# Kernel optimization log

Hardware: AMD Instinct MI355X
Metric: run time of the kernel (lower is better)

The kernel has to match this reference:

```python
import jax, jax.numpy as jnp
import numpy as np

B, C, LO, LQ, H = 64, 4, 64, 128, 768
NEG = -10000.0


def _trilinear(u, um, v, vm, w1, b1, w2, b2, w3):
    # u: [N, Lu, H], v: [N, Lv, H]; returns [N, Lu, Lv]
    p1 = u @ w1 + b1                                  # [N, Lu, 1]
    p2 = (v @ w2 + b2).transpose(0, 2, 1)             # [N, 1, Lv]
    p3 = jnp.einsum('bud,bvd->buv', u * w3, v)        # trilinear term
    return p1 + p2 + p3 + ((1.0 - um) * NEG)[:, :, None] + ((1.0 - vm) * NEG)[:, None, :]


def _forward(encoded_o, encoded_q, om, qm,
             att_W1_w, att_W1_b, att_W2_w, att_W2_b, att_W3,
             Wc_self_w, Wc_self_b, Wc_w, Wc_b, Va_w, Va_b, Wg_w, Wg_b,
             co_W1_w, co_W1_b, co_W2_w, co_W2_b, co_W3, Wp_w, Wp_b,
             sa_W1_w, sa_W1_b, sa_W2_w, sa_W2_b, sa_W3, Wf_w, Wf_b):
    b, c, lo, h = encoded_o.shape
    lq = encoded_q.shape[2]
    p = c * (c - 1)
    # ---- pairwise option-compare (OCN_Att_layer) over all (i, j), j != i ----
    i_idx = np.repeat(np.arange(c), c - 1)
    j_idx = np.array([j for i in range(c) for j in range(c) if j != i])
    o_i = encoded_o[:, i_idx].reshape(b * p, lo, h)   # 'ok'
    o_j = encoded_o[:, j_idx].reshape(b * p, lo, h)   # 'ol'
    m_i = om[:, i_idx].reshape(b * p, lo)
    m_j = om[:, j_idx].reshape(b * p, lo)
    A = _trilinear(o_j, m_j, o_i, m_i, att_W1_w, att_W1_b, att_W2_w, att_W2_b, att_W3)
    att = jax.nn.softmax(A, axis=1)
    olk_ctx = jnp.einsum('bud,buv->bvd', o_j, att)    # [BP, LO, H]
    OLK = jnp.concatenate([o_i - olk_ctx, o_i * olk_ctx], axis=-1)  # [BP, LO, 2H]
    cmp_proj = OLK @ Wc_w + Wc_b                      # Wc applied per compare pair
    cmp_sum = cmp_proj.reshape(b, c, c - 1, lo, h).sum(axis=2).reshape(b * c, lo, h)
    # ---- merge layer (per candidate, flattened into batch) ----
    o1 = encoded_o.reshape(b * c, lo, h)
    q = encoded_q.reshape(b * c, lq, h)
    omf = om.reshape(b * c, lo)
    qmf = qm.reshape(b * c, lq)
    Aq = jax.nn.softmax(q @ Va_w + Va_b + ((1.0 - qmf) * NEG)[:, :, None], axis=1)  # [BC, LQ, 1]
    Q = jnp.einsum('bld,blo->bod', q, Aq)             # [BC, 1, H]
    OCK = jnp.tanh(o1 @ Wc_self_w + Wc_self_b + cmp_sum)
    Qb = jnp.broadcast_to(Q, (b * c, lo, h))
    G = jax.nn.sigmoid(jnp.concatenate([o1, OCK, Qb], axis=-1) @ Wg_w + Wg_b)
    merged = G * o1 + (1.0 - G) * OCK                 # [BC, LO, H]
    # ---- co-attention with question ----
    A2 = _trilinear(q, qmf, merged, omf, co_W1_w, co_W1_b, co_W2_w, co_W2_b, co_W3)  # [BC, LQ, LO]
    ACK = jax.nn.softmax(A2, axis=2)
    OA = jnp.einsum('bqo,bod->bqd', ACK, merged)      # [BC, LQ, H]
    APK = jax.nn.softmax(A2, axis=1)
    dOA = jnp.concatenate([q, OA], axis=-1)           # [BC, LQ, 2H]
    POAA = jnp.einsum('bqd,bqo->bod', dOA, APK)       # [BC, LO, 2H]
    OPK = jax.nn.relu(jnp.concatenate([merged, POAA], axis=-1) @ Wp_w + Wp_b)
    # ---- self-attention ----
    A3 = _trilinear(OPK, omf, OPK, omf, sa_W1_w, sa_W1_b, sa_W2_w, sa_W2_b, sa_W3)
    att3 = jax.nn.softmax(A3, axis=1)
    OSK = jnp.einsum('bud,buv->bvd', OPK, att3)
    OFK = jax.nn.relu(jnp.concatenate([OPK, OSK, OPK - OSK, OPK * OSK], axis=-1) @ Wf_w + Wf_b)
    return OFK.reshape(b, c, lo, h).max(axis=2)       # [B, C, H]


def setup_inputs():
    ks = jax.random.split(jax.random.key(0), 32)
    def p(i, shape, s=0.02):
        return jax.random.normal(ks[i], shape, jnp.float32) * s
    return {
        'encoded_o': jax.random.normal(ks[0], (B, C, LO, H), jnp.float32),
        'encoded_q': jax.random.normal(ks[1], (B, C, LQ, H), jnp.float32),
        'option_mask': jnp.ones((B, C, LO), jnp.int32),
        'question_mask': jnp.ones((B, C, LQ), jnp.int32),
        'att_W1_w': p(2, (H, 1)), 'att_W1_b': p(3, (1,)),
        'att_W2_w': p(4, (H, 1)), 'att_W2_b': p(5, (1,)),
        'att_W3': p(6, (H,)),
        'Wc_self_w': p(7, (H, H)), 'Wc_self_b': p(8, (H,)),
        'Wc_w': p(9, (2 * H, H)), 'Wc_b': p(10, (H,)),
        'Va_w': p(11, (H, 1)), 'Va_b': p(12, (1,)),
        'Wg_w': p(13, (3 * H, H)), 'Wg_b': p(14, (H,)),
        'co_W1_w': p(15, (H, 1)), 'co_W1_b': p(16, (1,)),
        'co_W2_w': p(17, (H, 1)), 'co_W2_b': p(18, (1,)),
        'co_W3': p(19, (H,)),
        'Wp_w': p(20, (3 * H, H)), 'Wp_b': p(21, (H,)),
        'sa_W1_w': p(22, (H, 1)), 'sa_W1_b': p(23, (1,)),
        'sa_W2_w': p(24, (H, 1)), 'sa_W2_b': p(25, (1,)),
        'sa_W3': p(26, (H,)),
        'Wf_w': p(27, (4 * H, H)), 'Wf_b': p(28, (H,)),
    }


def reference(encoded_o, encoded_q, option_mask, question_mask,
              att_W1_w, att_W1_b, att_W2_w, att_W2_b, att_W3,
              Wc_self_w, Wc_self_b, Wc_w, Wc_b, Va_w, Va_b, Wg_w, Wg_b,
              co_W1_w, co_W1_b, co_W2_w, co_W2_b, co_W3, Wp_w, Wp_b,
              sa_W1_w, sa_W1_b, sa_W2_w, sa_W2_b, sa_W3, Wf_w, Wf_b):
    return _forward(encoded_o, encoded_q,
                    option_mask.astype(jnp.float32), question_mask.astype(jnp.float32),
                    att_W1_w, att_W1_b, att_W2_w, att_W2_b, att_W3,
                    Wc_self_w, Wc_self_b, Wc_w, Wc_b, Va_w, Va_b, Wg_w, Wg_b,
                    co_W1_w, co_W1_b, co_W2_w, co_W2_b, co_W3, Wp_w, Wp_b,
                    sa_W1_w, sa_W1_b, sa_W2_w, sa_W2_b, sa_W3, Wf_w, Wf_b)
```

## Files before the change

kernel.cpp:

```cpp
#include <hip/hip_runtime.h>
#include <math.h>


#define NEGC (-10000.0f)
constexpr int HD = 768;
constexpr int KSTR = 9216;

constexpr int EP_TANH = 1;
constexpr int EP_MERGE = 2;
constexpr int EP_RELU = 3;
constexpr int EP_RELU_MAX = 4;

typedef __attribute__((ext_vector_type(8))) short bf16x8;
typedef __attribute__((ext_vector_type(8))) unsigned short u16x8;
typedef __attribute__((ext_vector_type(4))) unsigned short u16x4;
typedef __attribute__((ext_vector_type(4))) float f32x4;

__device__ inline void st8(float* dst, float4 a0, float4 a1) {
  dst[0] = a0.x; dst[1] = a0.y; dst[2] = a0.z; dst[3] = a0.w;
  dst[4] = a1.x; dst[5] = a1.y; dst[6] = a1.z; dst[7] = a1.w;
}

__device__ inline unsigned short f2bf(float x) {
  unsigned int u = __float_as_uint(x);
  u += 0x7fffu + ((u >> 16) & 1u);
  return (unsigned short)(u >> 16);
}

__device__ inline float bf2f(unsigned short u) {
  return __uint_as_float(((unsigned int)u) << 16);
}

__device__ inline u16x8 pack8(float4 a, float4 b) {
  u16x8 r;
  r[0] = f2bf(a.x); r[1] = f2bf(a.y); r[2] = f2bf(a.z); r[3] = f2bf(a.w);
  r[4] = f2bf(b.x); r[5] = f2bf(b.y); r[6] = f2bf(b.z); r[7] = f2bf(b.w);
  return r;
}

__device__ inline u16x4 pack4(float4 a) {
  u16x4 r;
  r[0] = f2bf(a.x); r[1] = f2bf(a.y); r[2] = f2bf(a.z); r[3] = f2bf(a.w);
  return r;
}

__device__ inline void gload_lds16(const unsigned short* src, unsigned short* dst) {
  __builtin_amdgcn_global_load_lds(
      (const __attribute__((address_space(1))) void*)src,
      (__attribute__((address_space(3))) void*)dst, 16, 0, 0);
}

__global__ __launch_bounds__(256)
void bfprep_dot_kernel(const float* __restrict__ x, const float* __restrict__ w3,
                       const float* __restrict__ w1, const float* __restrict__ b1,
                       const float* __restrict__ w2, const float* __restrict__ b2,
                       unsigned short* __restrict__ xbf, unsigned short* __restrict__ xw3,
                       float* __restrict__ o1, float* __restrict__ o2, int ntok) {
  int tok = blockIdx.x * 4 + (threadIdx.x >> 6);
  int lane = threadIdx.x & 63;
  if (tok >= ntok) return;
  const float* xp = x + (size_t)tok * HD;
  unsigned short* xb = xbf + (size_t)tok * HD;
  unsigned short* xw = xw3 + (size_t)tok * HD;
  float s1 = 0.f, s2 = 0.f;
#pragma unroll
  for (int i = 0; i < 3; ++i) {
    int c = (lane + (i << 6)) << 2;
    float4 xv = *(const float4*)(xp + c);
    float4 w3v = *(const float4*)(w3 + c);
    float4 wa = *(const float4*)(w1 + c);
    float4 wb = *(const float4*)(w2 + c);
    s1 = fmaf(xv.x, wa.x, s1); s1 = fmaf(xv.y, wa.y, s1);
    s1 = fmaf(xv.z, wa.z, s1); s1 = fmaf(xv.w, wa.w, s1);
    s2 = fmaf(xv.x, wb.x, s2); s2 = fmaf(xv.y, wb.y, s2);
    s2 = fmaf(xv.z, wb.z, s2); s2 = fmaf(xv.w, wb.w, s2);
    *(u16x4*)(xb + c) = pack4(xv);
    float4 sv;
    sv.x = xv.x * w3v.x; sv.y = xv.y * w3v.y; sv.z = xv.z * w3v.z; sv.w = xv.w * w3v.w;
    *(u16x4*)(xw + c) = pack4(sv);
  }
#pragma unroll
  for (int off = 32; off; off >>= 1) {
    s1 += __shfl_xor(s1, off);
    s2 += __shfl_xor(s2, off);
  }
  if (lane == 0) { o1[tok] = s1 + b1[0]; o2[tok] = s2 + b2[0]; }
}

__global__ __launch_bounds__(256)
void opkprep_kernel(const unsigned short* __restrict__ x, const float* __restrict__ w3,
                    const float* __restrict__ w1, const float* __restrict__ b1,
                    const float* __restrict__ w2, const float* __restrict__ b2,
                    unsigned short* __restrict__ xw3,
                    float* __restrict__ o1, float* __restrict__ o2, int ntok) {
  int tok = blockIdx.x * 4 + (threadIdx.x >> 6);
  int lane = threadIdx.x & 63;
  if (tok >= ntok) return;
  const unsigned short* xp = x + (size_t)tok * HD;
  unsigned short* xw = xw3 + (size_t)tok * HD;
  float s1 = 0.f, s2 = 0.f;
#pragma unroll
  for (int i = 0; i < 3; ++i) {
    int c = (lane + (i << 6)) << 2;
    u16x4 xv = *(const u16x4*)(xp + c);
    float x0 = bf2f(xv[0]), x1 = bf2f(xv[1]), x2 = bf2f(xv[2]), x3 = bf2f(xv[3]);
    float4 w3v = *(const float4*)(w3 + c);
    float4 wa = *(const float4*)(w1 + c);
    float4 wb = *(const float4*)(w2 + c);
    s1 = fmaf(x0, wa.x, s1); s1 = fmaf(x1, wa.y, s1);
    s1 = fmaf(x2, wa.z, s1); s1 = fmaf(x3, wa.w, s1);
    s2 = fmaf(x0, wb.x, s2); s2 = fmaf(x1, wb.y, s2);
    s2 = fmaf(x2, wb.z, s2); s2 = fmaf(x3, wb.w, s2);
    u16x4 sv;
    sv[0] = f2bf(x0 * w3v.x); sv[1] = f2bf(x1 * w3v.y);
    sv[2] = f2bf(x2 * w3v.z); sv[3] = f2bf(x3 * w3v.w);
    *(u16x4*)(xw + c) = sv;
  }
#pragma unroll
  for (int off = 32; off; off >>= 1) {
    s1 += __shfl_xor(s1, off);
    s2 += __shfl_xor(s2, off);
  }
  if (lane == 0) { o1[tok] = s1 + b1[0]; o2[tok] = s2 + b2[0]; }
}

__global__ __launch_bounds__(256)
void dot768_bf16(const unsigned short* __restrict__ x,
                 const float* __restrict__ w1, const float* __restrict__ b1,
                 float* __restrict__ o1, int ntok) {
  int tok = blockIdx.x * 4 + (threadIdx.x >> 6);
  int lane = threadIdx.x & 63;
  if (tok >= ntok) return;
  const unsigned short* xp = x + (size_t)tok * HD;
  float s1 = 0.f;
#pragma unroll
  for (int i = 0; i < 3; ++i) {
    int c = (lane + (i << 6)) << 2;
    u16x4 xv = *(const u16x4*)(xp + c);
    float4 wa = *(const float4*)(w1 + c);
    s1 = fmaf(bf2f(xv[0]), wa.x, s1); s1 = fmaf(bf2f(xv[1]), wa.y, s1);
    s1 = fmaf(bf2f(xv[2]), wa.z, s1); s1 = fmaf(bf2f(xv[3]), wa.w, s1);
  }
#pragma unroll
  for (int off = 32; off; off >>= 1) s1 += __shfl_xor(s1, off);
  if (lane == 0) o1[tok] = s1 + b1[0];
}

__global__ void bias_ock_kernel(const float* __restrict__ b1, const float* __restrict__ b2,
                                float* __restrict__ o) {
  int n = blockIdx.x * 256 + threadIdx.x;
  if (n < HD) o[n] = b1[n] + 3.f * b2[n];
}

__global__ __launch_bounds__(256)
void qpool2_kernel(const float* __restrict__ q,
                   const float* __restrict__ Va_w, const float* __restrict__ Va_b,
                   const float* __restrict__ coW1_w, const float* __restrict__ coW1_b,
                   const int* __restrict__ qm,
                   float* __restrict__ qco1, float* __restrict__ Q) {
  __shared__ float qa_s[128];
  __shared__ float wgt[128];
  __shared__ float wred[4];
  const int t = threadIdx.x, bc = blockIdx.x;
  const int lane = t & 63, wv = t >> 6;
  const float* qb = q + (size_t)bc * (128 * HD);
  for (int it = 0; it < 32; ++it) {
    const int tl = it * 4 + wv;
    const float* xp = qb + (size_t)tl * HD;
    float s1 = 0.f, s2 = 0.f;
#pragma unroll
    for (int i = 0; i < 3; ++i) {
      int c = (lane + (i << 6)) << 2;
      float4 xv = *(const float4*)(xp + c);
      float4 wa = *(const float4*)(Va_w + c);
      float4 wb = *(const float4*)(coW1_w + c);
      s1 = fmaf(xv.x, wa.x, s1); s1 = fmaf(xv.y, wa.y, s1);
      s1 = fmaf(xv.z, wa.z, s1); s1 = fmaf(xv.w, wa.w, s1);
      s2 = fmaf(xv.x, wb.x, s2); s2 = fmaf(xv.y, wb.y, s2);
      s2 = fmaf(xv.z, wb.z, s2); s2 = fmaf(xv.w, wb.w, s2);
    }
#pragma unroll
    for (int off = 32; off; off >>= 1) {
      s1 += __shfl_xor(s1, off);
      s2 += __shfl_xor(s2, off);
    }
    if (lane == 0) {
      qa_s[tl] = s1 + Va_b[0];
      qco1[bc * 128 + tl] = s2 + coW1_b[0];
    }
  }
  __syncthreads();
  const int* qmp = qm + bc * 128;
  float v = -1e30f;
  if (t < 128) v = qa_s[t] + (1.f - (float)qmp[t]) * NEGC;
  float m = v;
#pragma unroll
  for (int off = 32; off; off >>= 1) m = fmaxf(m, __shfl_xor(m, off));
  if ((t & 63) == 0) wred[t >> 6] = m;
  __syncthreads();
  float gm = fmaxf(fmaxf(wred[0], wred[1]), fmaxf(wred[2], wred[3]));
  float e = (t < 128) ? expf(v - gm) : 0.f;
  float s = e;
#pragma unroll
  for (int off = 32; off; off >>= 1) s += __shfl_xor(s, off);
  __syncthreads();
  if ((t & 63) == 0) wred[t >> 6] = s;
  __syncthreads();
  float tot = wred[0] + wred[1] + wred[2] + wred[3];
  if (t < 128) wgt[t] = e / tot;
  __syncthreads();
  float* Qp = Q + (size_t)bc * HD;
  for (int d = t; d < HD; d += 256) {
    float acc = 0.f;
    for (int l = 0; l < 128; ++l) acc = fmaf(wgt[l], qb[(size_t)l * HD + d], acc);
    Qp[d] = acc;
  }
}

template<int NJ>
__global__ __launch_bounds__(256)
void p1_kernel(const unsigned short* __restrict__ Xbf, const unsigned short* __restrict__ Xw3,
               const float* __restrict__ s1g, const float* __restrict__ s2g,
               const int* __restrict__ maskg, unsigned short* __restrict__ PtG) {
  __shared__ __align__(16) unsigned short Ua[64 * 136];
  __shared__ __align__(16) unsigned short Vb[64 * 136];
  __shared__ float Sbuf[64][66];
  __shared__ float red[4][64];
  const int t = threadIdx.x;
  int ubc, vbc;
  if (NJ == 1) {
    ubc = vbc = blockIdx.x;
  } else {
    const int b = blockIdx.x / 12, pr = blockIdx.x % 12;
    const int i = pr / 3, jj = pr % 3;
    const int j = jj + (jj >= i ? 1 : 0);
    vbc = (b << 2) + i; ubc = (b << 2) + j;
  }
  const unsigned short* U = Xbf + (size_t)ubc * (64 * HD);
  const unsigned short* V = Xw3 + (size_t)vbc * (64 * HD);
  const int w = t >> 6, lane = t & 63, l15 = lane & 15, l4 = lane >> 4;
  const int srow = t >> 2, scol = (t & 3) << 5;
  f32x4 acc[4] = {};
  for (int k0 = 0; k0 < HD; k0 += 128) {
    const unsigned short* up = U + (size_t)srow * HD + k0 + scol;
    const unsigned short* vp = V + (size_t)srow * HD + k0 + scol;
    unsigned short* ua = &Ua[srow * 136 + scol];
    unsigned short* vb = &Vb[srow * 136 + scol];
#pragma unroll
    for (int z = 0; z < 4; ++z) {
      *(u16x8*)(ua + z * 8) = *(const u16x8*)(up + z * 8);
      *(u16x8*)(vb + z * 8) = *(const u16x8*)(vp + z * 8);
    }
    __syncthreads();
#pragma unroll
    for (int ks = 0; ks < 4; ++ks) {
      bf16x8 af = *(const bf16x8*)(&Ua[(w * 16 + l15) * 136 + ks * 32 + l4 * 8]);
#pragma unroll
      for (int n = 0; n < 4; ++n) {
        bf16x8 bf = *(const bf16x8*)(&Vb[(n * 16 + l15) * 136 + ks * 32 + l4 * 8]);
        acc[n] = __builtin_amdgcn_mfma_f32_16x16x32_bf16(af, bf, acc[n], 0, 0, 0);
      }
    }
    __syncthreads();
  }
  {
    float s1v[4];
#pragma unroll
    for (int r = 0; r < 4; ++r) {
      int u = w * 16 + l4 * 4 + r;
      s1v[r] = s1g[ubc * 64 + u] + (1.f - (float)maskg[ubc * 64 + u]) * NEGC;
    }
#pragma unroll
    for (int n = 0; n < 4; ++n) {
      int v = n * 16 + l15;
      float s2v = s2g[vbc * 64 + v] + (1.f - (float)maskg[vbc * 64 + v]) * NEGC;
#pragma unroll
      for (int r = 0; r < 4; ++r)
        Sbuf[w * 16 + l4 * 4 + r][v] = acc[n][r] + s1v[r] + s2v;
    }
  }
  __syncthreads();
  {
    const int v = t & 63, part = t >> 6;
    float m = -1e30f;
#pragma unroll
    for (int z = 0; z < 16; ++z) m = fmaxf(m, Sbuf[part * 16 + z][v]);
    red[part][v] = m;
    __syncthreads();
    float gm = fmaxf(fmaxf(red[0][v], red[1][v]), fmaxf(red[2][v], red[3][v]));
    float s = 0.f;
#pragma unroll
    for (int z = 0; z < 16; ++z) {
      float e = expf(Sbuf[part * 16 + z][v] - gm);
      Sbuf[part * 16 + z][v] = e;
      s += e;
    }
    __syncthreads();
    red[part][v] = s;
    __syncthreads();
    float cinv = 1.f / (red[0][v] + red[1][v] + red[2][v] + red[3][v]);
    unsigned short* pt = PtG + (size_t)blockIdx.x * 4096 + v * 64 + part * 16;
#pragma unroll
    for (int z = 0; z < 16; ++z) pt[z] = f2bf(Sbuf[part * 16 + z][v] * cinv);
  }
}

template<int NJ>
__global__ __launch_bounds__(256)
void p2_kernel(const unsigned short* __restrict__ Xbf, const unsigned short* __restrict__ PtG,
               const unsigned short* __restrict__ Oi,
               unsigned short* __restrict__ osk,
               unsigned short* __restrict__ y1, unsigned short* __restrict__ y2) {
  __shared__ __align__(16) unsigned short Pts[NJ][64 * 72];
  __shared__ __align__(16) unsigned short U2[64 * 192];
  const int t = threadIdx.x;
  const int dq = blockIdx.x, bc = blockIdx.y;
  const int d0 = dq * 192;
  const int b = bc >> 2, i = bc & 3;
  const int w = t >> 6, lane = t & 63, l15 = lane & 15, l4 = lane >> 4;
  {
    const int v = t >> 2, cs = (t & 3) << 4;
#pragma unroll
    for (int jj = 0; jj < NJ; ++jj) {
      size_t src = (NJ == 1 ? (size_t)bc : (size_t)(b * 12 + i * 3 + jj)) * 4096 + v * 64 + cs;
      *(u16x8*)(&Pts[jj][v * 72 + cs]) = *(const u16x8*)(PtG + src);
      *(u16x8*)(&Pts[jj][v * 72 + cs + 8]) = *(const u16x8*)(PtG + src + 8);
    }
  }
  f32x4 acc[4][3] = {};
  const int su = t >> 2, sc0 = (t & 3) * 48;
  const int sswz = ((su >> 3) & 3) << 5;
  for (int jj = 0; jj < NJ; ++jj) {
    const int ubc = (NJ == 1) ? bc : ((b << 2) + (jj + (jj >= i ? 1 : 0)));
    __syncthreads();
    {
      const unsigned short* up = Xbf + (size_t)ubc * (64 * HD) + (size_t)su * HD + d0 + sc0;
#pragma unroll
      for (int it = 0; it < 6; ++it) {
        u16x8 vdat = *(const u16x8*)(up + it * 8);
        *(u16x8*)((char*)U2 + ((su * 384 + (sc0 + it * 8) * 2) ^ sswz)) = vdat;
      }
    }
    __syncthreads();
    const unsigned short* ptj = &Pts[jj][0];
#pragma unroll
    for (int ks = 0; ks < 2; ++ks) {
      bf16x8 bfr[3];
#pragma unroll
      for (int n = 0; n < 3; ++n) {
        const int col = (w * 3 + n) * 16 + l15;
#pragma unroll
        for (int e = 0; e < 8; ++e) {
          const int uk = ks * 32 + l4 * 8 + e;
          const int byte = (uk * 384 + col * 2) ^ (((uk >> 3) & 3) << 5);
          bfr[n][e] = *(const short*)((const char*)U2 + byte);
        }
      }
#pragma unroll
      for (int m = 0; m < 4; ++m) {
        bf16x8 af = *(const bf16x8*)(ptj + (m * 16 + l15) * 72 + ks * 32 + l4 * 8);
#pragma unroll
        for (int n = 0; n < 3; ++n)
          acc[m][n] = __builtin_amdgcn_mfma_f32_16x16x32_bf16(af, bfr[n], acc[m][n], 0, 0, 0);
      }
    }
  }
  const unsigned short* oip = Oi + (size_t)bc * (64 * HD);
  const size_t obase = (size_t)bc * (64 * HD);
#pragma unroll
  for (int m = 0; m < 4; ++m)
#pragma unroll
    for (int n = 0; n < 3; ++n) {
      const int d = d0 + (w * 3 + n) * 16 + l15;
#pragma unroll
      for (int r = 0; r < 4; ++r) {
        const int v = m * 16 + l4 * 4 + r;
        const size_t idx = obase + (size_t)v * HD + d;
        const float cs = acc[m][n][r];
        const float oi = bf2f(oip[(size_t)v * HD + d]);
        if (NJ == 3) {
          y1[idx] = f2bf(fmaf(3.f, oi, -cs));
          y2[idx] = f2bf(oi * cs);
        } else {
          osk[idx] = f2bf(cs);
          y1[idx] = f2bf(oi - cs);
          y2[idx] = f2bf(oi * cs);
        }
      }
    }
}

__global__ __launch_bounds__(256)
void poaa2_kernel(const float* __restrict__ qin, const unsigned short* __restrict__ mergedb,
                  const float* __restrict__ qco1, const float* __restrict__ ms2,
                  const int* __restrict__ qm, const int* __restrict__ om,
                  const float* __restrict__ w3,
                  unsigned short* __restrict__ PLO, unsigned short* __restrict__ PHI) {
  __shared__ __align__(16) char smem[77312];
  __shared__ float red[4][64];
  __shared__ float rowm[128], rowfac[128];
  __shared__ float colfac[64];
  __shared__ float gmax_s;
  float* T = (float*)smem;
  unsigned short* Aq = (unsigned short*)smem;
  unsigned short* Bm = (unsigned short*)(smem + 18432);
  unsigned short* Tt = (unsigned short*)(smem + 33280);
  unsigned short* Tft = (unsigned short*)(smem + 50688);
  unsigned short* M2bf = (unsigned short*)(smem + 68096);
  unsigned short* Qc = (unsigned short*)smem;
  unsigned short* Mc = (unsigned short*)(smem + 18432);

  const int t = threadIdx.x, dqh = blockIdx.x, bc = blockIdx.y;
  const int w = t >> 6, lane = t & 63, l15 = lane & 15, l4 = lane >> 4;
  const float* qp = qin + (size_t)bc * (128 * HD);
  const unsigned short* mp = mergedb + (size_t)bc * (64 * HD);
  const float* qc = qco1 + bc * 128;
  const int* qmp = qm + bc * 128;
  const float* msp = ms2 + bc * 64;
  const int* omp = om + bc * 64;

  {
    const int arow = t >> 1, acs = (t & 1) << 5;
    const int brow = t >> 2, bcs = (t & 3) << 4;
    f32x4 acc[2][4] = {};
    for (int k0 = 0; k0 < HD; k0 += 64) {
      {
        const float* p = qp + (size_t)arow * HD + k0 + acs;
        const float* wp = w3 + k0 + acs;
        unsigned short* dst = &Aq[arow * 72 + acs];
#pragma unroll
        for (int z = 0; z < 4; ++z) {
          float4 a = *(const float4*)(p + z * 8);
          float4 b = *(const float4*)(p + z * 8 + 4);
          float4 wa = *(const float4*)(wp + z * 8);
          float4 wb = *(const float4*)(wp + z * 8 + 4);
          a.x *= wa.x; a.y *= wa.y; a.z *= wa.z; a.w *= wa.w;
          b.x *= wb.x; b.y *= wb.y; b.z *= wb.z; b.w *= wb.w;
          *(u16x8*)(dst + z * 8) = pack8(a, b);
        }
      }
      {
        const unsigned short* p = mp + (size_t)brow * HD + k0 + bcs;
        unsigned short* dst = &Bm[brow * 72 + bcs];
        *(u16x8*)(dst) = *(const u16x8*)(p);
        *(u16x8*)(dst + 8) = *(const u16x8*)(p + 8);
      }
      __syncthreads();
#pragma unroll
      for (int ks = 0; ks < 2; ++ks) {
        bf16x8 af[2], bf[4];
#pragma unroll
        for (int m = 0; m < 2; ++m)
          af[m] = *(const bf16x8*)(&Aq[(w * 32 + m * 16 + l15) * 72 + ks * 32 + l4 * 8]);
#pragma unroll
        for (int n = 0; n < 4; ++n)
          bf[n] = *(const bf16x8*)(&Bm[(n * 16 + l15) * 72 + ks * 32 + l4 * 8]);
#pragma unroll
        for (int m = 0; m < 2; ++m)
#pragma unroll
          for (int n = 0; n < 4; ++n)
            acc[m][n] = __builtin_amdgcn_mfma_f32_16x16x32_bf16(af[m], bf[n], acc[m][n], 0, 0, 0);
      }
      __syncthreads();
    }
#pragma unroll
    for (int n = 0; n < 4; ++n) {
      const int v = n * 16 + l15;
      const float ct = msp[v] + (1.f - (float)omp[v]) * NEGC;
#pragma unroll
      for (int m = 0; m < 2; ++m)
#pragma unroll
        for (int r = 0; r < 4; ++r) {
          const int qrow = w * 32 + m * 16 + l4 * 4 + r;
          const float rt = qc[qrow] + (1.f - (float)qmp[qrow]) * NEGC;
          T[qrow * 65 + v] = acc[m][n][r] + rt + ct;
        }
    }
  }
  __syncthreads();
  {
    int qrow = t >> 1, h = t & 1;
    float m = -1e30f;
    for (int v = h * 32; v < h * 32 + 32; ++v) m = fmaxf(m, T[qrow * 65 + v]);
    m = fmaxf(m, __shfl_xor(m, 1));
    float s = 0.f;
    for (int v = h * 32; v < h * 32 + 32; ++v) s += expf(T[qrow * 65 + v] - m);
    s += __shfl_xor(s, 1);
    if (h == 0) { rowm[qrow] = m; rowfac[qrow] = s; }
  }
  float colm_loc = 0.f;
  {
    int v = t & 63, part = t >> 6;
    float m = -1e30f;
    for (int qq = part * 32; qq < part * 32 + 32; ++qq) m = fmaxf(m, T[qq * 65 + v]);
    red[part][v] = m;
    __syncthreads();
    float cm = fmaxf(fmaxf(red[0][v], red[1][v]), fmaxf(red[2][v], red[3][v]));
    float s = 0.f;
    for (int qq = part * 32; qq < part * 32 + 32; ++qq) s += expf(T[qq * 65 + v] - cm);
    __syncthreads();
    red[part][v] = s;
    __syncthreads();
    if (part == 0) { colm_loc = cm; colfac[v] = red[0][v] + red[1][v] + red[2][v] + red[3][v]; }
  }
  __syncthreads();
  if (t < 64) {
    float m = fmaxf(rowm[t], rowm[t + 64]);
#pragma unroll
    for (int off = 32; off; off >>= 1) m = fmaxf(m, __shfl_xor(m, off));
    if (t == 0) gmax_s = m;
  }
  __syncthreads();
  const float gmax = gmax_s;
  if (t < 128) rowfac[t] = expf(fminf(gmax - rowm[t], 60.f)) / rowfac[t];
  if (t < 64) colfac[t] = expf(fminf(gmax - colm_loc, 60.f)) / colfac[t];
  __syncthreads();
  {
    const int o = t >> 2, qs = (t & 3) << 5;
    for (int z = 0; z < 32; ++z) {
      const int qq = qs + z;
      float e = expf(T[qq * 65 + o] - gmax);
      Tt[o * 136 + qq] = f2bf(e);
      Tft[o * 136 + qq] = f2bf(e * rowfac[qq]);
    }
  }
  __syncthreads();
  {
    f32x4 m2acc[4] = {};
#pragma unroll
    for (int ks = 0; ks < 4; ++ks) {
      bf16x8 af = *(const bf16x8*)(&Tt[(w * 16 + l15) * 136 + ks * 32 + l4 * 8]);
#pragma unroll
      for (int n = 0; n < 4; ++n) {
        bf16x8 bf = *(const bf16x8*)(&Tft[(n * 16 + l15) * 136 + ks * 32 + l4 * 8]);
        m2acc[n] = __builtin_amdgcn_mfma_f32_16x16x32_bf16(af, bf, m2acc[n], 0, 0, 0);
      }
    }
#pragma unroll
    for (int n = 0; n < 4; ++n)
#pragma unroll
      for (int r = 0; r < 4; ++r) {
        const int o = w * 16 + l4 * 4 + r;
        M2bf[o * 72 + n * 16 + l15] = f2bf(colfac[o] * m2acc[n][r]);
      }
  }
  const int dql = t >> 1, dqs = (t & 1) << 5;
  const int dml = t >> 2, dms = (t & 3) << 4;
  const int swq = ((dql >> 3) & 3) << 5;
  const int swm = ((dml >> 3) & 3) << 5;
  unsigned short* plo = PLO + (size_t)bc * (64 * HD);
  unsigned short* phi = PHI + (size_t)bc * (64 * HD);
  for (int dc = dqh * 6; dc < dqh * 6 + 6; ++dc) {
    const int d0 = dc * 64;
    __syncthreads();
    {
      const float* p = qp + (size_t)dql * HD + d0 + dqs;
#pragma unroll
      for (int z = 0; z < 4; ++z) {
        float4 a = *(const float4*)(p + z * 8);
        float4 b = *(const float4*)(p + z * 8 + 4);
        *(u16x8*)((char*)Qc + ((dql * 144 + (dqs + z * 8) * 2) ^ swq)) = pack8(a, b);
      }
    }
    {
      const unsigned short* p = mp + (size_t)dml * HD + d0 + dms;
      *(u16x8*)((char*)Mc + ((dml * 144 + dms * 2) ^ swm)) = *(const u16x8*)p;
      *(u16x8*)((char*)Mc + ((dml * 144 + (dms + 8) * 2) ^ swm)) = *(const u16x8*)(p + 8);
    }
    __syncthreads();
    const int col = w * 16 + l15;
    f32x4 lacc[4] = {};
#pragma unroll
    for (int ks = 0; ks < 4; ++ks) {
      bf16x8 bf;
#pragma unroll
      for (int e = 0; e < 8; ++e) {
        const int qq = ks * 32 + l4 * 8 + e;
        bf[e] = *(const short*)((const char*)Qc + ((qq * 144 + col * 2) ^ (((qq >> 3) & 3) << 5)));
      }
#pragma unroll
      for (int m = 0; m < 4; ++m) {
        bf16x8 af = *(const bf16x8*)(&Tt[(m * 16 + l15) * 136 + ks * 32 + l4 * 8]);
        lacc[m] = __builtin_amdgcn_mfma_f32_16x16x32_bf16(af, bf, lacc[m], 0, 0, 0);
      }
    }
    f32x4 pacc[4] = {};
#pragma unroll
    for (int ks = 0; ks < 2; ++ks) {
      bf16x8 bf;
#pragma unroll
      for (int e = 0; e < 8; ++e) {
        const int vv = ks * 32 + l4 * 8 + e;
        bf[e] = *(const short*)((const char*)Mc + ((vv * 144 + col * 2) ^ (((vv >> 3) & 3) << 5)));
      }
#pragma unroll
      for (int m = 0; m < 4; ++m) {
        bf16x8 af = *(const bf16x8*)(&M2bf[(m * 16 + l15) * 72 + ks * 32 + l4 * 8]);
        pacc[m] = __builtin_amdgcn_mfma_f32_16x16x32_bf16(af, bf, pacc[m], 0, 0, 0);
      }
    }
#pragma unroll
    for (int m = 0; m < 4; ++m)
#pragma unroll
      for (int r = 0; r < 4; ++r) {
        const int o = m * 16 + l4 * 4 + r;
        const int d = d0 + w * 16 + l15;
        plo[(size_t)o * HD + d] = f2bf(colfac[o] * lacc[m][r]);
        phi[(size_t)o * HD + d] = f2bf(pacc[m][r]);
      }
  }
}

struct GemmArgs {
  const float* a[4];
  const float* w[4];
  int nchunks;
  const float* bias;
  float* out;
};

__global__ __launch_bounds__(256)
void gemm_store_kernel(GemmArgs g) {
  __shared__ float As[64][33];
  __shared__ float Ws[32][65];
  const int t = threadIdx.x;
  const int m0 = blockIdx.y << 6, n0 = blockIdx.x << 6;
  const int tr = t >> 4, tc = t & 15;
  float acc[4][4];
#pragma unroll
  for (int x = 0; x < 4; ++x)
#pragma unroll
    for (int y = 0; y < 4; ++y) acc[x][y] = 0.f;
  const int arow = t >> 2, acs = (t & 3) << 3;
  const int wrow = t >> 3, wcs = (t & 7) << 3;
  for (int c = 0; c < g.nchunks; ++c) {
    const float* Ap = g.a[c] + (size_t)(m0 + arow) * HD + acs;
    const float* Wp = g.w[c] + (size_t)wrow * HD + n0 + wcs;
    for (int k0 = 0; k0 < HD; k0 += 32) {
      float4 a0 = *(const float4*)(Ap + k0);
      float4 a1 = *(const float4*)(Ap + k0 + 4);
      st8(&As[arow][acs], a0, a1);
      float4 w0 = *(const float4*)(Wp + (size_t)k0 * HD);
      float4 w1 = *(const float4*)(Wp + (size_t)k0 * HD + 4);
      st8(&Ws[wrow][wcs], w0, w1);
      __syncthreads();
#pragma unroll
      for (int kk = 0; kk < 32; ++kk) {
        float av[4], bv[4];
#pragma unroll
        for (int x = 0; x < 4; ++x) av[x] = As[(tr << 2) + x][kk];
#pragma unroll
        for (int y = 0; y < 4; ++y) bv[y] = Ws[kk][(tc << 2) + y];
#pragma unroll
        for (int x = 0; x < 4; ++x)
#pragma unroll
          for (int y = 0; y < 4; ++y) acc[x][y] = fmaf(av[x], bv[y], acc[x][y]);
      }
      __syncthreads();
    }
  }
#pragma unroll
  for (int x = 0; x < 4; ++x) {
    const int r = m0 + (tr << 2) + x;
#pragma unroll
    for (int y = 0; y < 4; ++y) {
      const int n = n0 + (tc << 2) + y;
      g.out[(size_t)r * HD + n] = acc[x][y] + g.bias[n];
    }
  }
}

struct WcAllArgs {
  const float* src[12];
  int basecol[12];
  unsigned short* dst;
};

__global__ __launch_bounds__(256)
void wconv_all_kernel(WcAllArgs g) {
  __shared__ float tile[64][65];
  const int slice = blockIdx.y;
  const float* src = g.src[slice];
  const int bi = blockIdx.x % 12, bj = blockIdx.x / 12;
  const int t = threadIdx.x;
  const int r = t >> 2, cseg = (t & 3) << 4;
  const float* p = src + (size_t)(bi * 64 + r) * HD + bj * 64 + cseg;
#pragma unroll
  for (int j = 0; j < 16; j += 4) {
    float4 v = *(const float4*)(p + j);
    tile[r][cseg + j + 0] = v.x; tile[r][cseg + j + 1] = v.y;
    tile[r][cseg + j + 2] = v.z; tile[r][cseg + j + 3] = v.w;
  }
  __syncthreads();
  unsigned short* q = g.dst + (size_t)(bj * 64 + r) * KSTR + g.basecol[slice] + bi * 64 + cseg;
  u16x8 lo, hi;
#pragma unroll
  for (int j = 0; j < 8; ++j) lo[j] = f2bf(tile[cseg + j][r]);
#pragma unroll
  for (int j = 0; j < 8; ++j) hi[j] = f2bf(tile[cseg + 8 + j][r]);
  *(u16x8*)q = lo;
  *(u16x8*)(q + 8) = hi;
}

struct MMArgs {
  const unsigned short* a[4];
  int K;
  const unsigned short* wt;
  const float* bias;
  const unsigned short* aux0;
  const unsigned short* aux1;
  const float* aux2;
  float* outf;
  unsigned short* outb;
};

template<int EP>
__global__ __launch_bounds__(256)
void mfma_gemm_kernel(MMArgs g) {
  __shared__ __align__(16) unsigned short As[3][128 * 32];
  __shared__ __align__(16) unsigned short Bs[3][128 * 32];
  const int t = threadIdx.x;
  const int lane = t & 63, w = t >> 6;
  const int wr = w >> 1, wc = w & 1;
  const int m0 = blockIdx.x << 7, n0 = blockIdx.y << 7;
  const int l15 = lane & 15, l4 = lane >> 4;
  f32x4 acc[4][4] = {};

  const int srow = w * 32 + (lane >> 2);
  const int gcol = (((lane & 3) ^ ((lane >> 3) & 3))) * 8;
  const int rsw = (l15 >> 1) & 3;
  const int rcol = ((l4 ^ rsw)) * 8;

  const int nkt = g.K >> 5;

  auto issue = [&](int kt, int buf) {
    const int c = kt / 24;
    const int koff = (kt - c * 24) << 5;
    const unsigned short* ap = g.a[c] + (size_t)(m0 + srow) * HD + koff + gcol;
    const unsigned short* bp = g.wt + (size_t)(n0 + srow) * KSTR + (kt << 5) + gcol;
    gload_lds16(ap, &As[buf][w * 1024]);
    gload_lds16(ap + (size_t)16 * HD, &As[buf][w * 1024 + 512]);
    gload_lds16(bp, &Bs[buf][w * 1024]);
    gload_lds16(bp + (size_t)16 * KSTR, &Bs[buf][w * 1024 + 512]);
  };

  auto compute = [&](int kt, int buf, bool prefetch) {
    bf16x8 af[4], bfr[4];
#pragma unroll
    for (int mi = 0; mi < 4; ++mi)
      af[mi] = *(const bf16x8*)(&As[buf][(wr * 64 + mi * 16 + l15) * 32 + rcol]);
#pragma unroll
    for (int ni = 0; ni < 4; ++ni)
      bfr[ni] = *(const bf16x8*)(&Bs[buf][(wc * 64 + ni * 16 + l15) * 32 + rcol]);
    asm volatile("s_waitcnt lgkmcnt(0)" ::: "memory");
    __builtin_amdgcn_s_barrier();
    if (prefetch) issue(kt + 3, buf);
    __builtin_amdgcn_s_setprio(1);
#pragma unroll
    for (int mi = 0; mi < 4; ++mi)
#pragma unroll
      for (int ni = 0; ni < 4; ++ni)
        acc[mi][ni] = __builtin_amdgcn_mfma_f32_16x16x32_bf16(af[mi], bfr[ni], acc[mi][ni], 0, 0, 0);
    __builtin_amdgcn_s_setprio(0);
  };

  issue(0, 0); issue(1, 1); issue(2, 2);
  int buf = 0;
  int kt = 0;
  for (; kt < nkt - 2; ++kt) {
    asm volatile("s_waitcnt vmcnt(8)" ::: "memory");
    __builtin_amdgcn_s_barrier();
    compute(kt, buf, kt + 3 < nkt);
    buf = (buf == 2) ? 0 : buf + 1;
  }
  asm volatile("s_waitcnt vmcnt(4)" ::: "memory");
  __builtin_amdgcn_s_barrier();
  compute(kt, buf, false);
  buf = (buf == 2) ? 0 : buf + 1;
  ++kt;
  asm volatile("s_waitcnt vmcnt(0)" ::: "memory");
  __builtin_amdgcn_s_barrier();
  compute(kt, buf, false);

  if (EP == EP_RELU_MAX) {
#pragma unroll
    for (int ni = 0; ni < 4; ++ni) {
      const int n = n0 + wc * 64 + ni * 16 + l15;
      const float b = g.bias[n];
      float m = 0.f;
#pragma unroll
      for (int mi = 0; mi < 4; ++mi)
#pragma unroll
        for (int r = 0; r < 4; ++r)
          m = fmaxf(m, acc[mi][ni][r] + b);
      m = fmaxf(m, 0.f);
      m = fmaxf(m, __shfl_xor(m, 16));
      m = fmaxf(m, __shfl_xor(m, 32));
      if (l4 == 0) g.outf[(size_t)((m0 >> 6) + wr) * HD + n] = m;
    }
  } else {
#pragma unroll
    for (int mi = 0; mi < 4; ++mi)
#pragma unroll
      for (int r = 0; r < 4; ++r) {
        const int row = m0 + wr * 64 + mi * 16 + l4 * 4 + r;
#pragma unroll
        for (int ni = 0; ni < 4; ++ni) {
          const int n = n0 + wc * 64 + ni * 16 + l15;
          const size_t oi = (size_t)row * HD + n;
          float v = acc[mi][ni][r];
          if (EP == EP_TANH) {
            g.outb[oi] = f2bf(tanhf(v + g.bias[n]));
          } else if (EP == EP_MERGE) {
            float gg = v + g.aux2[(size_t)(row >> 6) * HD + n];
            float sg = 1.f / (1.f + expf(-gg));
            float o1v = bf2f(g.aux0[oi]);
            float ock = bf2f(g.aux1[oi]);
            g.outb[oi] = f2bf(fmaf(sg, o1v - ock, ock));
          } else {
            g.outb[oi] = f2bf(fmaxf(v + g.bias[n], 0.f));
          }
        }
      }
  }
}

extern "C" void kernel_launch(void* const* d_in, const int* in_sizes, int n_in,
                              void* d_out, int out_size, void* d_ws, size_t ws_size,
                              hipStream_t stream) {
  const float* enc_o = (const float*)d_in[0];
  const float* enc_q = (const float*)d_in[1];
  const int* om = (const int*)d_in[2];
  const int* qm = (const int*)d_in[3];
  const float* att_W1_w = (const float*)d_in[4];
  const float* att_W1_b = (const float*)d_in[5];
  const float* att_W2_w = (const float*)d_in[6];
  const float* att_W2_b = (const float*)d_in[7];
  const float* att_W3 = (const float*)d_in[8];
  const float* Wc_self_w = (const float*)d_in[9];
  const float* Wc_self_b = (const float*)d_in[10];
  const float* Wc_w = (const float*)d_in[11];
  const float* Wc_b = (const float*)d_in[12];
  const float* Va_w = (const float*)d_in[13];
  const float* Va_b = (const float*)d_in[14];
  const float* Wg_w = (const float*)d_in[15];
  const float* Wg_b = (const float*)d_in[16];
  const float* co_W1_w = (const float*)d_in[17];
  const float* co_W1_b = (const float*)d_in[18];
  const float* co_W2_w = (const float*)d_in[19];
  const float* co_W2_b = (const float*)d_in[20];
  const float* co_W3 = (const float*)d_in[21];
  const float* Wp_w = (const float*)d_in[22];
  const float* Wp_b = (const float*)d_in[23];
  const float* sa_W1_w = (const float*)d_in[24];
  const float* sa_W1_b = (const float*)d_in[25];
  const float* sa_W2_w = (const float*)d_in[26];
  const float* sa_W2_b = (const float*)d_in[27];
  const float* sa_W3 = (const float*)d_in[28];
  const float* Wf_w = (const float*)d_in[29];
  const float* Wf_b = (const float*)d_in[30];
  float* out = (float*)d_out;

  const int NTOK_O = 16384;
  const int HH = 768 * 768;

  float* ws = (float*)d_ws;
  size_t off = 0;
  auto carve = [&](size_t n) { float* p = ws + off; off += n; return p; };
  float* s1o   = carve(16384);
  float* s2o   = carve(16384);
  float* qco1  = carve(32768);
  float* ms2   = carve(16384);
  float* sa1   = carve(16384);
  float* sa2   = carve(16384);
  float* biasO = carve(1024);
  float* Qpool = carve(196608);
  float* Qg    = carve(196608);
  float* A2buf = carve(2097152);
  float* r1 = carve(12582912);
  float* r2 = carve(12582912);
  float* r3 = carve(12582912);
  float* r4 = carve(12582912);
  if (ws_size < off * sizeof(float)) return;
  unsigned short* OPKb  = (unsigned short*)r1;
  unsigned short* X1    = (unsigned short*)(r1 + 6291456);
  unsigned short* X3    = (unsigned short*)(r1 + 6291456);
  unsigned short* OCKb  = (unsigned short*)r2;
  unsigned short* PLOb  = (unsigned short*)r2;
  unsigned short* opkw3 = (unsigned short*)r2;
  unsigned short* X2    = (unsigned short*)(r2 + 6291456);
  unsigned short* MRGb  = (unsigned short*)r3;
  unsigned short* OSKb  = (unsigned short*)r3;
  unsigned short* X4    = (unsigned short*)(r3 + 6291456);
  unsigned short* eobf  = (unsigned short*)r4;
  unsigned short* eow3  = (unsigned short*)(r4 + 6291456);
  unsigned short* PHIb  = (unsigned short*)r4;
  unsigned short* wall  = (unsigned short*)(r4 + 6291456);
  unsigned short* PtG   = (unsigned short*)A2buf;

  const dim3 GBIG(128, 6);

  bfprep_dot_kernel<<<NTOK_O / 4, 256, 0, stream>>>(enc_o, att_W3, att_W1_w, att_W1_b,
                                                    att_W2_w, att_W2_b, eobf, eow3,
                                                    s1o, s2o, NTOK_O);
  qpool2_kernel<<<256, 256, 0, stream>>>(enc_q, Va_w, Va_b, co_W1_w, co_W1_b,
                                         qm, qco1, Qpool);
  bias_ock_kernel<<<3, 256, 0, stream>>>(Wc_self_b, Wc_b, biasO);

  p1_kernel<3><<<768, 256, 0, stream>>>(eobf, eow3, s1o, s2o, om, PtG);
  {
    WcAllArgs wa{};
    wa.src[0] = Wc_self_w; wa.src[1] = Wc_w;        wa.src[2] = Wc_w + HH;
    wa.src[3] = Wg_w;      wa.src[4] = Wg_w + HH;
    wa.src[5] = Wp_w;      wa.src[6] = Wp_w + HH;   wa.src[7] = Wp_w + 2 * HH;
    wa.src[8] = Wf_w;      wa.src[9] = Wf_w + HH;   wa.src[10] = Wf_w + 2 * HH;
    wa.src[11] = Wf_w + 3 * HH;
    int bases[12] = {0, 768, 1536, 2304, 3072, 3840, 4608, 5376, 6144, 6912, 7680, 8448};
    for (int i = 0; i < 12; ++i) wa.basecol[i] = bases[i];
    wa.dst = wall;
    wconv_all_kernel<<<dim3(144, 12), 256, 0, stream>>>(wa);
  }
  p2_kernel<3><<<dim3(4, 256), 256, 0, stream>>>(eobf, PtG, eobf, nullptr, X1, X2);

  {
    MMArgs g{};
    g.a[0] = eobf; g.a[1] = X1; g.a[2] = X2;
    g.K = 2304; g.wt = wall + 0; g.bias = biasO; g.outb = OCKb;
    mfma_gemm_kernel<EP_TANH><<<GBIG, 256, 0, stream>>>(g);
  }

  {
    GemmArgs g{};
    g.a[0] = Qpool; g.w[0] = Wg_w + 2 * HH;
    g.nchunks = 1; g.bias = Wg_b; g.out = Qg;
    gemm_store_kernel<<<dim3(12, 4), 256, 0, stream>>>(g);
  }

  {
    MMArgs g{};
    g.a[0] = eobf; g.a[1] = OCKb;
    g.K = 1536; g.wt = wall + 2304; g.bias = nullptr;
    g.aux0 = eobf; g.aux1 = OCKb; g.aux2 = Qg; g.outb = MRGb;
    mfma_gemm_kernel<EP_MERGE><<<GBIG, 256, 0, stream>>>(g);
  }

  dot768_bf16<<<NTOK_O / 4, 256, 0, stream>>>(MRGb, co_W2_w, co_W2_b, ms2, NTOK_O);
  poaa2_kernel<<<dim3(2, 256), 256, 0, stream>>>(enc_q, MRGb, qco1, ms2, qm, om,
                                                 co_W3, PLOb, PHIb);

  {
    MMArgs g{};
    g.a[0] = MRGb; g.a[1] = PLOb; g.a[2] = PHIb;
    g.K = 2304; g.wt = wall + 3840; g.bias = Wp_b; g.outb = OPKb;
    mfma_gemm_kernel<EP_RELU><<<GBIG, 256, 0, stream>>>(g);
  }

  opkprep_kernel<<<NTOK_O / 4, 256, 0, stream>>>(OPKb, sa_W3, sa_W1_w, sa_W1_b,
                                                 sa_W2_w, sa_W2_b, opkw3, sa1, sa2, NTOK_O);
  p1_kernel<1><<<256, 256, 0, stream>>>(OPKb, opkw3, sa1, sa2, om, PtG);
  p2_kernel<1><<<dim3(4, 256), 256, 0, stream>>>(OPKb, PtG, OPKb, OSKb, X3, X4);

  {
    MMArgs g{};
    g.a[0] = OPKb; g.a[1] = OSKb; g.a[2] = X3; g.a[3] = X4;
    g.K = 3072; g.wt = wall + 6144; g.bias = Wf_b; g.outf = out;
    mfma_gemm_kernel<EP_RELU_MAX><<<GBIG, 256, 0, stream>>>(g);
  }
}
```

Before: 609.4 us.

## Fuse ms2 dot and OCK bias into consumers; restructure GEMM k-loop pipeline

Removes the dot768_bf16 kernel by computing the co_W2 projection of merged rows inside poaa2 while staging the B tile, reducing the partial sums via shuffles into shared memory. Drops bias_ock_kernel by folding bias + 3*bias2 into the tanh epilogue. Also rewrites the mfma GEMM main loop from a three-deep prefetch (vmcnt 8) to issuing two ahead, with the barrier and next issue placed before the LDS reads. This saves two launches and some memory traffic, but prefetch depth drops, which can expose more load latency in the large GEMMs.

After: 687.4 us. 1.13x slower.

```diff
diff --git a/kernel.cpp b/kernel.cpp
--- a/kernel.cpp
+++ b/kernel.cpp
@@ -122,34 +122,6 @@
     s2 += __shfl_xor(s2, off);
   }
   if (lane == 0) { o1[tok] = s1 + b1[0]; o2[tok] = s2 + b2[0]; }
-}
-
-__global__ __launch_bounds__(256)
-void dot768_bf16(const unsigned short* __restrict__ x,
-                 const float* __restrict__ w1, const float* __restrict__ b1,
-                 float* __restrict__ o1, int ntok) {
-  int tok = blockIdx.x * 4 + (threadIdx.x >> 6);
-  int lane = threadIdx.x & 63;
-  if (tok >= ntok) return;
-  const unsigned short* xp = x + (size_t)tok * HD;
-  float s1 = 0.f;
-#pragma unroll
-  for (int i = 0; i < 3; ++i) {
-    int c = (lane + (i << 6)) << 2;
-    u16x4 xv = *(const u16x4*)(xp + c);
-    float4 wa = *(const float4*)(w1 + c);
-    s1 = fmaf(bf2f(xv[0]), wa.x, s1); s1 = fmaf(bf2f(xv[1]), wa.y, s1);
-    s1 = fmaf(bf2f(xv[2]), wa.z, s1); s1 = fmaf(bf2f(xv[3]), wa.w, s1);
-  }
-#pragma unroll
-  for (int off = 32; off; off >>= 1) s1 += __shfl_xor(s1, off);
-  if (lane == 0) o1[tok] = s1 + b1[0];
-}
-
-__global__ void bias_ock_kernel(const float* __restrict__ b1, const float* __restrict__ b2,
-                                float* __restrict__ o) {
-  int n = blockIdx.x * 256 + threadIdx.x;
-  if (n < HD) o[n] = b1[n] + 3.f * b2[n];
 }
 
 __global__ __launch_bounds__(256)
@@ -392,7 +364,8 @@
 
 __global__ __launch_bounds__(256)
 void poaa2_kernel(const float* __restrict__ qin, const unsigned short* __restrict__ mergedb,
-                  const float* __restrict__ qco1, const float* __restrict__ ms2,
+                  const float* __restrict__ qco1,
+                  const float* __restrict__ coW2_w, const float* __restrict__ coW2_b,
                   const int* __restrict__ qm, const int* __restrict__ om,
                   const float* __restrict__ w3,
                   unsigned short* __restrict__ PLO, unsigned short* __restrict__ PHI) {
@@ -400,6 +373,7 @@
   __shared__ float red[4][64];
   __shared__ float rowm[128], rowfac[128];
   __shared__ float colfac[64];
+  __shared__ float ms2_s[64];
   __shared__ float gmax_s;
   float* T = (float*)smem;
   unsigned short* Aq = (unsigned short*)smem;
@@ -416,13 +390,13 @@
   const unsigned short* mp = mergedb + (size_t)bc * (64 * HD);
   const float* qc = qco1 + bc * 128;
   const int* qmp = qm + bc * 128;
-  const float* msp = ms2 + bc * 64;
   const int* omp = om + bc * 64;
 
   {
     const int arow = t >> 1, acs = (t & 1) << 5;
     const int brow = t >> 2, bcs = (t & 3) << 4;
     f32x4 acc[2][4] = {};
+    float msacc = 0.f;
     for (int k0 = 0; k0 < HD; k0 += 64) {
       {
         const float* p = qp + (size_t)arow * HD + k0 + acs;
@@ -442,8 +416,23 @@
       {
         const unsigned short* p = mp + (size_t)brow * HD + k0 + bcs;
         unsigned short* dst = &Bm[brow * 72 + bcs];
-        *(u16x8*)(dst) = *(const u16x8*)(p);
-        *(u16x8*)(dst + 8) = *(const u16x8*)(p + 8);
+        u16x8 v0 = *(const u16x8*)(p);
+        u16x8 v1 = *(const u16x8*)(p + 8);
+        *(u16x8*)(dst) = v0;
+        *(u16x8*)(dst + 8) = v1;
+        const float* wp = coW2_w + k0 + bcs;
+        float4 wa = *(const float4*)(wp);
+        float4 wb = *(const float4*)(wp + 4);
+        float4 wc = *(const float4*)(wp + 8);
+        float4 wd = *(const float4*)(wp + 12);
+        msacc = fmaf(bf2f(v0[0]), wa.x, msacc); msacc = fmaf(bf2f(v0[1]), wa.y, msacc);
+        msacc = fmaf(bf2f(v0[2]), wa.z, msacc); msacc = fmaf(bf2f(v0[3]), wa.w, msacc);
+        msacc = fmaf(bf2f(v0[4]), wb.x, msacc); msacc = fmaf(bf2f(v0[5]), wb.y, msacc);
+        msacc = fmaf(bf2f(v0[6]), wb.z, msacc); msacc = fmaf(bf2f(v0[7]), wb.w, msacc);
+        msacc = fmaf(bf2f(v1[0]), wc.x, msacc); msacc = fmaf(bf2f(v1[1]), wc.y, msacc);
+        msacc = fmaf(bf2f(v1[2]), wc.z, msacc); msacc = fmaf(bf2f(v1[3]), wc.w, msacc);
+        msacc = fmaf(bf2f(v1[4]), wd.x, msacc); msacc = fmaf(bf2f(v1[5]), wd.y, msacc);
+        msacc = fmaf(bf2f(v1[6]), wd.z, msacc); msacc = fmaf(bf2f(v1[7]), wd.w, msacc);
       }
       __syncthreads();
 #pragma unroll
@@ -463,10 +452,14 @@
       }
       __syncthreads();
     }
+    msacc += __shfl_xor(msacc, 1);
+    msacc += __shfl_xor(msacc, 2);
+    if ((t & 3) == 0) ms2_s[brow] = msacc + coW2_b[0];
+    __syncthreads();
 #pragma unroll
     for (int n = 0; n < 4; ++n) {
       const int v = n * 16 + l15;
-      const float ct = msp[v] + (1.f - (float)omp[v]) * NEGC;
+      const float ct = ms2_s[v] + (1.f - (float)omp[v]) * NEGC;
 #pragma unroll
       for (int m = 0; m < 2; ++m)
 #pragma unroll
@@ -707,6 +700,7 @@
   int K;
   const unsigned short* wt;
   const float* bias;
+  const float* bias2;
   const unsigned short* aux0;
   const unsigned short* aux1;
   const float* aux2;
@@ -744,7 +738,15 @@
     gload_lds16(bp + (size_t)16 * KSTR, &Bs[buf][w * 1024 + 512]);
   };
 
-  auto compute = [&](int kt, int buf, bool prefetch) {
+  issue(0, 0); issue(1, 1);
+  int buf = 0;
+  for (int kt = 0; kt < nkt; ++kt) {
+    if (kt < nkt - 1)
+      asm volatile("s_waitcnt vmcnt(4)" ::: "memory");
+    else
+      asm volatile("s_waitcnt vmcnt(0)" ::: "memory");
+    __builtin_amdgcn_s_barrier();
+    if (kt + 2 < nkt) issue(kt + 2, (kt + 2) % 3);
     bf16x8 af[4], bfr[4];
 #pragma unroll
     for (int mi = 0; mi < 4; ++mi)
@@ -753,8 +755,6 @@
     for (int ni = 0; ni < 4; ++ni)
       bfr[ni] = *(const bf16x8*)(&Bs[buf][(wc * 64 + ni * 16 + l15) * 32 + rcol]);
     asm volatile("s_waitcnt lgkmcnt(0)" ::: "memory");
-    __builtin_amdgcn_s_barrier();
-    if (prefetch) issue(kt + 3, buf);
     __builtin_amdgcn_s_setprio(1);
 #pragma unroll
     for (int mi = 0; mi < 4; ++mi)
@@ -762,25 +762,8 @@
       for (int ni = 0; ni < 4; ++ni)
         acc[mi][ni] = __builtin_amdgcn_mfma_f32_16x16x32_bf16(af[mi], bfr[ni], acc[mi][ni], 0, 0, 0);
     __builtin_amdgcn_s_setprio(0);
-  };
-
-  issue(0, 0); issue(1, 1); issue(2, 2);
-  int buf = 0;
-  int kt = 0;
-  for (; kt < nkt - 2; ++kt) {
-    asm volatile("s_waitcnt vmcnt(8)" ::: "memory");
-    __builtin_amdgcn_s_barrier();
-    compute(kt, buf, kt + 3 < nkt);
     buf = (buf == 2) ? 0 : buf + 1;
   }
-  asm volatile("s_waitcnt vmcnt(4)" ::: "memory");
-  __builtin_amdgcn_s_barrier();
-  compute(kt, buf, false);
-  buf = (buf == 2) ? 0 : buf + 1;
-  ++kt;
-  asm volatile("s_waitcnt vmcnt(0)" ::: "memory");
-  __builtin_amdgcn_s_barrier();
-  compute(kt, buf, false);
 
   if (EP == EP_RELU_MAX) {
 #pragma unroll
@@ -810,7 +793,7 @@
           const size_t oi = (size_t)row * HD + n;
           float v = acc[mi][ni][r];
           if (EP == EP_TANH) {
-            g.outb[oi] = f2bf(tanhf(v + g.bias[n]));
+            g.outb[oi] = f2bf(tanhf(v + g.bias[n] + 3.f * g.bias2[n]));
           } else if (EP == EP_MERGE) {
             float gg = v + g.aux2[(size_t)(row >> 6) * HD + n];
             float sg = 1.f / (1.f + expf(-gg));
@@ -870,10 +853,8 @@
   float* s1o   = carve(16384);
   float* s2o   = carve(16384);
   float* qco1  = carve(32768);
-  float* ms2   = carve(16384);
   float* sa1   = carve(16384);
   float* sa2   = carve(16384);
-  float* biasO = carve(1024);
   float* Qpool = carve(196608);
   float* Qg    = carve(196608);
   float* A2buf = carve(2097152);
@@ -905,7 +886,6 @@
                                                     s1o, s2o, NTOK_O);
   qpool2_kernel<<<256, 256, 0, stream>>>(enc_q, Va_w, Va_b, co_W1_w, co_W1_b,
                                          qm, qco1, Qpool);
-  bias_ock_kernel<<<3, 256, 0, stream>>>(Wc_self_b, Wc_b, biasO);
 
   p1_kernel<3><<<768, 256, 0, stream>>>(eobf, eow3, s1o, s2o, om, PtG);
   {
@@ -925,7 +905,8 @@
   {
     MMArgs g{};
     g.a[0] = eobf; g.a[1] = X1; g.a[2] = X2;
-    g.K = 2304; g.wt = wall + 0; g.bias = biasO; g.outb = OCKb;
+    g.K = 2304; g.wt = wall + 0;
+    g.bias = Wc_self_b; g.bias2 = Wc_b; g.outb = OCKb;
     mfma_gemm_kernel<EP_TANH><<<GBIG, 256, 0, stream>>>(g);
   }
 
@@ -944,9 +925,8 @@
     mfma_gemm_kernel<EP_MERGE><<<GBIG, 256, 0, stream>>>(g);
   }
 
-  dot768_bf16<<<NTOK_O / 4, 256, 0, stream>>>(MRGb, co_W2_w, co_W2_b, ms2, NTOK_O);
-  poaa2_kernel<<<dim3(2, 256), 256, 0, stream>>>(enc_q, MRGb, qco1, ms2, qm, om,
-                                                 co_W3, PLOb, PHIb);
+  poaa2_kernel<<<dim3(2, 256), 256, 0, stream>>>(enc_q, MRGb, qco1, co_W2_w, co_W2_b,
+                                                 qm, om, co_W3, PLOb, PHIb);
 
   {
     MMArgs g{};
```
